# Kernel tuning notes

Measured on AMD Instinct MI355X. Metric: run time of the kernel, lower is better.

## Reference

```python
import jax, jax.numpy as jnp
import numpy as np

D_MODEL = 1024
NUM_HEADS = 16
HEAD_DIM = D_MODEL // NUM_HEADS
THETA = 10000.0
B, S = 2, 2048


def setup_inputs() -> dict:
    key = jax.random.key(0)
    ks = jax.random.split(key, 9)
    std = 1.0 / np.sqrt(D_MODEL)
    x = jax.random.normal(ks[0], (B, S, D_MODEL), dtype=jnp.float32)
    Wq = jax.random.normal(ks[1], (D_MODEL, D_MODEL), dtype=jnp.float32) * std
    Wk = jax.random.normal(ks[2], (D_MODEL, D_MODEL), dtype=jnp.float32) * std
    Wv = jax.random.normal(ks[3], (D_MODEL, D_MODEL), dtype=jnp.float32) * std
    Wo = jax.random.normal(ks[4], (D_MODEL, D_MODEL), dtype=jnp.float32) * std
    bq = jax.random.normal(ks[5], (D_MODEL,), dtype=jnp.float32) * std
    bk = jax.random.normal(ks[6], (D_MODEL,), dtype=jnp.float32) * std
    bv = jax.random.normal(ks[7], (D_MODEL,), dtype=jnp.float32) * std
    bo = jax.random.normal(ks[8], (D_MODEL,), dtype=jnp.float32) * std
    return {"x": x, "Wq": Wq, "bq": bq, "Wk": Wk, "bk": bk,
            "Wv": Wv, "bv": bv, "Wo": Wo, "bo": bo}


def _apply_rope(t, cos, sin):
    # t: [B, H, S, hd]; cos/sin: [S, hd//2]; interleaved-pair rotation
    t1 = t[..., 0::2]
    t2 = t[..., 1::2]
    r1 = t1 * cos - t2 * sin
    r2 = t1 * sin + t2 * cos
    return jnp.stack([r1, r2], axis=-1).reshape(t.shape)


def reference(x, Wq, bq, Wk, bk, Wv, bv, Wo, bo):
    B_, S_, D = x.shape
    H, hd = NUM_HEADS, HEAD_DIM
    # QKV projections (nn.Linear: x @ W.T + b)
    q = (x @ Wq.T + bq).reshape(B_, S_, H, hd).transpose(0, 2, 1, 3)  # [B,H,S,hd]
    k = (x @ Wk.T + bk).reshape(B_, S_, H, hd).transpose(0, 2, 1, 3)
    v = (x @ Wv.T + bv).reshape(B_, S_, H, hd).transpose(0, 2, 1, 3)
    # RoPE with token_positions = arange(S)
    pos = jnp.arange(S_, dtype=jnp.float32)
    inv_freq = 1.0 / (THETA ** (jnp.arange(0, hd, 2, dtype=jnp.float32) / hd))
    ang = pos[:, None] * inv_freq[None, :]  # [S, hd//2]
    cos, sin = jnp.cos(ang), jnp.sin(ang)
    q = _apply_rope(q, cos, sin)
    k = _apply_rope(k, cos, sin)
    # causal scaled-dot-product attention
    scores = jnp.einsum('bhqd,bhkd->bhqk', q, k) / jnp.sqrt(jnp.asarray(hd, x.dtype))
    causal = jnp.arange(S_)[:, None] >= jnp.arange(S_)[None, :]  # [S,S]
    scores = jnp.where(causal, scores, -jnp.inf)
    attn = jax.nn.softmax(scores, axis=-1)
    out = jnp.einsum('bhqk,bhkd->bhqd', attn, v)  # [B,H,S,hd]
    out = out.transpose(0, 2, 1, 3).reshape(B_, S_, D)
    return out @ Wo.T + bo
```

## Files before the change

### kernel.cpp

```cpp
#include <hip/hip_runtime.h>
#include <hip/hip_bf16.h>
#include <stdint.h>

typedef __bf16 bf16_t;
typedef __bf16 bf16x4 __attribute__((ext_vector_type(4)));
typedef __bf16 bf16x8 __attribute__((ext_vector_type(8)));
typedef float  f32x4  __attribute__((ext_vector_type(4)));

#define DM    1024
#define NH    16
#define HD    64
#define SEQ   2048
#define BATCH 2
#define BS    (BATCH*SEQ)
#define NQKV  (3*DM)

#define GLOAD_LDS16(g, l) \
  __builtin_amdgcn_global_load_lds((const __attribute__((address_space(1))) void*)(g), \
                                   (__attribute__((address_space(3))) void*)(l), 16, 0, 0)

__device__ __forceinline__ f32x4 mfma16(bf16x8 a, bf16x8 b, f32x4 c) {
  return __builtin_amdgcn_mfma_f32_16x16x32_bf16(a, b, c, 0, 0, 0);
}

__global__ __launch_bounds__(256) void k_cast_all(
    const float* __restrict__ x,  const float* __restrict__ Wq,
    const float* __restrict__ Wk, const float* __restrict__ Wv,
    const float* __restrict__ Wo, const float* __restrict__ bq,
    const float* __restrict__ bk, const float* __restrict__ bv,
    bf16_t* __restrict__ xb, bf16_t* __restrict__ Wcat,
    bf16_t* __restrict__ Wob, float* __restrict__ bcat,
    float2* __restrict__ rt)
{
  const int bid = blockIdx.x, tid = threadIdx.x;
  if (bid >= 4099) {
    const int idx = (bid - 4099) * 256 + tid;
    const int s = idx >> 5, i = idx & 31;
    float inv = powf(10000.0f, -(float)(2 * i) / 64.0f);
    float ang = (float)s * inv;
    rt[idx] = make_float2(cosf(ang), sinf(ang));
    return;
  }
  if (bid >= 4096) {
    const int k = bid - 4096;
    const float* src = (k == 0) ? bq : (k == 1) ? bk : bv;
    *(float4*)&bcat[k * DM + tid * 4] = *(const float4*)&src[tid * 4];
    return;
  }
  const float* src; bf16_t* dst; int i;
  if (bid < 2048)      { src = x;  dst = xb;                i = bid * 2048 + tid * 8; }
  else if (bid < 2560) { src = Wq; dst = Wcat;              i = (bid - 2048) * 2048 + tid * 8; }
  else if (bid < 3072) { src = Wk; dst = Wcat + DM * DM;    i = (bid - 2560) * 2048 + tid * 8; }
  else if (bid < 3584) { src = Wv; dst = Wcat + 2 * DM * DM;i = (bid - 3072) * 2048 + tid * 8; }
  else                 { src = Wo; dst = Wob;               i = (bid - 3584) * 2048 + tid * 8; }
  float4 a = *(const float4*)(src + i);
  float4 b = *(const float4*)(src + i + 4);
  bf16x8 o;
  o[0] = (bf16_t)a.x; o[1] = (bf16_t)a.y; o[2] = (bf16_t)a.z; o[3] = (bf16_t)a.w;
  o[4] = (bf16_t)b.x; o[5] = (bf16_t)b.y; o[6] = (bf16_t)b.z; o[7] = (bf16_t)b.w;
  *(bf16x8*)(dst + i) = o;
}

__global__ __launch_bounds__(256) void k_gemm_qk(
    const bf16_t* __restrict__ A, const bf16_t* __restrict__ B,
    const float* __restrict__ bias, const float2* __restrict__ rt,
    bf16_t* __restrict__ Qo, bf16_t* __restrict__ Ko)
{
  const int K = DM;
  __shared__ __align__(16) bf16_t As[128 * 32];
  __shared__ __align__(16) bf16_t Bs[128 * 32];
  const int tid  = threadIdx.x;
  const int lane = tid & 63;
  const int wave = tid >> 6;
  const int wr = wave >> 1, wc = wave & 1;
  const int m0 = blockIdx.y * 128, n0 = blockIdx.x * 128;
  const int c16 = lane & 15, g = lane >> 4;

  f32x4 acc[4][4];
  #pragma unroll
  for (int i = 0; i < 4; ++i)
    #pragma unroll
    for (int j = 0; j < 4; ++j)
      #pragma unroll
      for (int e = 0; e < 4; ++e) acc[i][j][e] = 0.0f;

  const int srow = wave * 32;
  const int lrow = lane >> 2;
  const int lk   = (lane & 3) * 8;
  const bf16_t* ga0 = A + (size_t)(m0 + srow +      lrow) * K + lk;
  const bf16_t* ga1 = A + (size_t)(m0 + srow + 16 + lrow) * K + lk;
  const bf16_t* gb0 = B + (size_t)(n0 + srow +      lrow) * K + lk;
  const bf16_t* gb1 = B + (size_t)(n0 + srow + 16 + lrow) * K + lk;
  bf16_t* la0 = &As[(srow)      * 32];
  bf16_t* la1 = &As[(srow + 16) * 32];
  bf16_t* lb0 = &Bs[(srow)      * 32];
  bf16_t* lb1 = &Bs[(srow + 16) * 32];

  const bf16_t* pa = &As[(wr * 64 + c16) * 32 + g * 8];
  const bf16_t* pb = &Bs[(wc * 64 + c16) * 32 + g * 8];

  for (int kt = 0; kt < K; kt += 32) {
    GLOAD_LDS16(ga0 + kt, la0);
    GLOAD_LDS16(ga1 + kt, la1);
    GLOAD_LDS16(gb0 + kt, lb0);
    GLOAD_LDS16(gb1 + kt, lb1);
    __syncthreads();
    bf16x8 af[4], bfr[4];
    #pragma unroll
    for (int t = 0; t < 4; ++t) af[t]  = *(const bf16x8*)(pa + t * 16 * 32);
    #pragma unroll
    for (int t = 0; t < 4; ++t) bfr[t] = *(const bf16x8*)(pb + t * 16 * 32);
    #pragma unroll
    for (int i = 0; i < 4; ++i)
      #pragma unroll
      for (int j = 0; j < 4; ++j)
        acc[i][j] = mfma16(bfr[j], af[i], acc[i][j]);
    __syncthreads();
  }

  const int region = n0 >> 10;
  bf16_t* dst = region ? Ko : Qo;
  const float qs = region ? 1.0f : (0.125f * 1.44269504088896f);
  #pragma unroll
  for (int j = 0; j < 4; ++j) {
    const int nb = n0 + wc * 64 + j * 16 + (g << 2);
    const float4 bv = *(const float4*)&bias[nb];
    const int h  = (nb >> 6) & 15;
    const int d0 = nb & 63;
    #pragma unroll
    for (int i = 0; i < 4; ++i) {
      const int m = m0 + wr * 64 + i * 16 + c16;
      const int s = m & 2047;
      const int bh = ((m >> 11) << 4) + h;
      const float4 cs = *(const float4*)&rt[(size_t)s * 32 + (d0 >> 1)];
      const float v0 = acc[i][j][0] + bv.x;
      const float v1 = acc[i][j][1] + bv.y;
      const float v2 = acc[i][j][2] + bv.z;
      const float v3 = acc[i][j][3] + bv.w;
      bf16x4 ov;
      ov[0] = (bf16_t)((v0 * cs.x - v1 * cs.y) * qs);
      ov[1] = (bf16_t)((v0 * cs.y + v1 * cs.x) * qs);
      ov[2] = (bf16_t)((v2 * cs.z - v3 * cs.w) * qs);
      ov[3] = (bf16_t)((v2 * cs.w + v3 * cs.z) * qs);
      *(bf16x4*)&dst[((size_t)bh * SEQ + s) * HD + d0] = ov;
    }
  }
}

__global__ __launch_bounds__(256) void k_gemm_v(
    const bf16_t* __restrict__ A, const bf16_t* __restrict__ B,
    const float* __restrict__ bias, bf16_t* __restrict__ Vt)
{
  const int K = DM;
  __shared__ __align__(16) bf16_t As[128 * 32];
  __shared__ __align__(16) bf16_t Bs[128 * 32];
  const int tid  = threadIdx.x;
  const int lane = tid & 63;
  const int wave = tid >> 6;
  const int wr = wave >> 1, wc = wave & 1;
  const int m0 = blockIdx.y * 128, n0 = blockIdx.x * 128;
  const int c16 = lane & 15, g = lane >> 4;

  f32x4 acc[4][4];
  #pragma unroll
  for (int i = 0; i < 4; ++i)
    #pragma unroll
    for (int j = 0; j < 4; ++j)
      #pragma unroll
      for (int e = 0; e < 4; ++e) acc[i][j][e] = 0.0f;

  const int srow = wave * 32;
  const int lrow = lane >> 2;
  const int lk   = (lane & 3) * 8;
  const bf16_t* ga0 = A + (size_t)(m0 + srow +      lrow) * K + lk;
  const bf16_t* ga1 = A + (size_t)(m0 + srow + 16 + lrow) * K + lk;
  const bf16_t* gb0 = B + (size_t)(n0 + srow +      lrow) * K + lk;
  const bf16_t* gb1 = B + (size_t)(n0 + srow + 16 + lrow) * K + lk;
  bf16_t* la0 = &As[(srow)      * 32];
  bf16_t* la1 = &As[(srow + 16) * 32];
  bf16_t* lb0 = &Bs[(srow)      * 32];
  bf16_t* lb1 = &Bs[(srow + 16) * 32];

  const bf16_t* pa = &As[(wr * 64 + c16) * 32 + g * 8];
  const bf16_t* pb = &Bs[(wc * 64 + c16) * 32 + g * 8];

  for (int kt = 0; kt < K; kt += 32) {
    GLOAD_LDS16(ga0 + kt, la0);
    GLOAD_LDS16(ga1 + kt, la1);
    GLOAD_LDS16(gb0 + kt, lb0);
    GLOAD_LDS16(gb1 + kt, lb1);
    __syncthreads();
    bf16x8 af[4], bfr[4];
    #pragma unroll
    for (int t = 0; t < 4; ++t) af[t]  = *(const bf16x8*)(pa + t * 16 * 32);
    #pragma unroll
    for (int t = 0; t < 4; ++t) bfr[t] = *(const bf16x8*)(pb + t * 16 * 32);
    #pragma unroll
    for (int i = 0; i < 4; ++i)
      #pragma unroll
      for (int j = 0; j < 4; ++j)
        acc[i][j] = mfma16(af[i], bfr[j], acc[i][j]);
    __syncthreads();
  }

  const int rbase = m0 + wr * 64 + (g << 2);
  const int cbase = n0 + wc * 64 + c16;
  #pragma unroll
  for (int j = 0; j < 4; ++j) {
    const int c = cbase + j * 16;
    const float bv = bias[c];
    const int h = (c >> 6) & 15;
    const int d = c & 63;
    #pragma unroll
    for (int i = 0; i < 4; ++i) {
      bf16x4 ov;
      #pragma unroll
      for (int e = 0; e < 4; ++e) ov[e] = (bf16_t)(acc[i][j][e] + bv);
      const int r0 = rbase + i * 16;
      const int bh = ((r0 >> 11) << 4) + h;
      const int s0 = r0 & 2047;
      const int u  = (s0 >> 4) & 3;
      const int p0 = (s0 & ~63) + ((u >> 1) << 5) + (g << 3) + ((u & 1) << 2);
      *(bf16x4*)&Vt[((size_t)bh * HD + d) * SEQ + p0] = ov;
    }
  }
}

__global__ __launch_bounds__(512) void k_gemm_out(
    const bf16_t* __restrict__ A, const bf16_t* __restrict__ B,
    const float* __restrict__ bias, float* __restrict__ C)
{
  const int K = DM, N = DM;
  __shared__ __align__(16) bf16_t As[128 * 32];
  __shared__ __align__(16) bf16_t Bs[128 * 32];
  const int tid  = threadIdx.x;
  const int lane = tid & 63;
  const int w    = tid >> 6;
  const int wr = w >> 2, wc = w & 3;
  const int m0 = blockIdx.y * 128, n0 = blockIdx.x * 128;
  const int c16 = lane & 15, g = lane >> 4;

  f32x4 acc[4][2];
  #pragma unroll
  for (int i = 0; i < 4; ++i)
    #pragma unroll
    for (int j = 0; j < 2; ++j)
      #pragma unroll
      for (int e = 0; e < 4; ++e) acc[i][j][e] = 0.0f;

  const int lrow = lane >> 2;
  const int lk   = (lane & 3) * 8;
  const bf16_t* ga = A + (size_t)(m0 + w * 16 + lrow) * K + lk;
  const bf16_t* gb = B + (size_t)(n0 + w * 16 + lrow) * K + lk;
  bf16_t* la = &As[(w * 16) * 32];
  bf16_t* lb = &Bs[(w * 16) * 32];

  const bf16_t* pa = &As[(wr * 64 + c16) * 32 + g * 8];
  const bf16_t* pb = &Bs[(wc * 32 + c16) * 32 + g * 8];

  for (int kt = 0; kt < K; kt += 32) {
    GLOAD_LDS16(ga + kt, la);
    GLOAD_LDS16(gb + kt, lb);
    __syncthreads();
    bf16x8 af[4], bfr[2];
    #pragma unroll
    for (int t = 0; t < 4; ++t) af[t]  = *(const bf16x8*)(pa + t * 16 * 32);
    #pragma unroll
    for (int t = 0; t < 2; ++t) bfr[t] = *(const bf16x8*)(pb + t * 16 * 32);
    #pragma unroll
    for (int i = 0; i < 4; ++i)
      #pragma unroll
      for (int j = 0; j < 2; ++j)
        acc[i][j] = mfma16(af[i], bfr[j], acc[i][j]);
    __syncthreads();
  }

  const int rbase = m0 + wr * 64 + (g << 2);
  const int cbase = n0 + wc * 32 + c16;
  #pragma unroll
  for (int j = 0; j < 2; ++j) {
    const int c = cbase + j * 16;
    const float bv = bias[c];
    #pragma unroll
    for (int i = 0; i < 4; ++i) {
      #pragma unroll
      for (int e = 0; e < 4; ++e) {
        const int r = rbase + i * 16 + e;
        C[(size_t)r * N + c] = acc[i][j][e] + bv;
      }
    }
  }
}

__global__ __launch_bounds__(256, 4) void k_attn(
    const bf16_t* __restrict__ Q, const bf16_t* __restrict__ K,
    const bf16_t* __restrict__ Vt, bf16_t* __restrict__ O)
{
  __shared__ __align__(16) bf16_t kbuf[2][64 * 64];
  __shared__ __align__(16) bf16_t vbuf[2][64 * 64];
  const int tid = threadIdx.x, lane = tid & 63, w = tid >> 6;
  const int rr = blockIdx.x >> 8;
  const int kk = (blockIdx.x >> 5) & 7;
  const int bh = blockIdx.x & 31;
  const int qt = (rr == 0) ? kk : (rr == 1) ? 15 - kk : (rr == 2) ? 16 + kk : 31 - kk;
  const int b  = bh >> 4, h = bh & 15;
  const int q0 = qt * 64 + w * 16;
  const int c16 = lane & 15;
  const int g   = lane >> 4;
  const int q   = q0 + c16;

  const bf16_t* Qb = Q  + (size_t)bh * SEQ * HD;
  const bf16_t* Kb = K  + (size_t)bh * SEQ * HD;
  const bf16_t* Vb = Vt + (size_t)bh * HD * SEQ;

  bf16x8 qf0 = *(const bf16x8*)&Qb[(size_t)q * HD + g * 8];
  bf16x8 qf1 = *(const bf16x8*)&Qb[(size_t)q * HD + 32 + g * 8];

  f32x4 oacc[4];
  #pragma unroll
  for (int dblk = 0; dblk < 4; ++dblk)
    #pragma unroll
    for (int e = 0; e < 4; ++e) oacc[dblk][e] = 0.0f;
  float m_ = -1e30f, l_ = 0.0f;

  const int ntile = qt + 1;

  const int soff0 = w * 1024 + lane * 16;
  const int soff1 = soff0 + 4096;
  const int srow0 = soff0 >> 7, srow1 = soff1 >> 7;
  const int scb0  = (soff0 & 127) ^ ((srow0 & 7) << 4);
  const int scb1  = (soff1 & 127) ^ ((srow1 & 7) << 4);
  const bf16_t* gk0 = &Kb[(size_t)srow0 * HD + (scb0 >> 1)];
  const bf16_t* gk1 = &Kb[(size_t)srow1 * HD + (scb1 >> 1)];
  const bf16_t* gv0 = &Vb[(size_t)srow0 * SEQ + (scb0 >> 1)];
  const bf16_t* gv1 = &Vb[(size_t)srow1 * SEQ + (scb1 >> 1)];
  bf16_t* lk0A = &kbuf[0][(w * 1024) >> 1];
  bf16_t* lk1A = &kbuf[0][(w * 1024 + 4096) >> 1];
  bf16_t* lk0B = &kbuf[1][(w * 1024) >> 1];
  bf16_t* lk1B = &kbuf[1][(w * 1024 + 4096) >> 1];
  bf16_t* lv0A = &vbuf[0][(w * 1024) >> 1];
  bf16_t* lv1A = &vbuf[0][(w * 1024 + 4096) >> 1];
  bf16_t* lv0B = &vbuf[1][(w * 1024) >> 1];
  bf16_t* lv1B = &vbuf[1][(w * 1024 + 4096) >> 1];

  const int sw = (c16 & 7) << 4;
  const int e0 = ((16 * g) ^ sw) >> 1;
  const int dhi = (((64 + 16 * g) ^ sw) >> 1) - e0;
  const bf16_t* kp0 = &kbuf[0][c16 * 64 + e0];
  const bf16_t* kp1 = &kbuf[1][c16 * 64 + e0];
  const bf16_t* vp0 = &vbuf[0][c16 * 64 + e0];
  const bf16_t* vp1 = &vbuf[1][c16 * 64 + e0];

  GLOAD_LDS16(gk0, lk0A); GLOAD_LDS16(gk1, lk1A);
  GLOAD_LDS16(gv0, lv0A); GLOAD_LDS16(gv1, lv1A);
  gk0 += 4096; gk1 += 4096; gv0 += 64; gv1 += 64;
  __syncthreads();

  for (int t = 0; t < ntile; ++t) {
    const bool odd = t & 1;
    if (t + 1 < ntile) {
      GLOAD_LDS16(gk0, odd ? lk0A : lk0B); GLOAD_LDS16(gk1, odd ? lk1A : lk1B);
      GLOAD_LDS16(gv0, odd ? lv0A : lv0B); GLOAD_LDS16(gv1, odd ? lv1A : lv1B);
      gk0 += 4096; gk1 += 4096; gv0 += 64; gv1 += 64;
    }

    const bf16_t* kp = odd ? kp1 : kp0;
    const bf16_t* vp = odd ? vp1 : vp0;

    f32x4 st[4];
    __builtin_amdgcn_s_setprio(1);
    #pragma unroll
    for (int u = 0; u < 4; ++u) {
      bf16x8 k0 = *(const bf16x8*)(kp + u * 1024);
      bf16x8 k1 = *(const bf16x8*)(kp + u * 1024 + dhi);
      f32x4 z; z[0] = z[1] = z[2] = z[3] = 0.0f;
      z = mfma16(k0, qf0, z);
      z = mfma16(k1, qf1, z);
      st[u] = z;
    }
    __builtin_amdgcn_s_setprio(0);

    bf16x8 vlo[4], vhi[4];
    #pragma unroll
    for (int dblk = 0; dblk < 4; ++dblk) {
      vlo[dblk] = *(const bf16x8*)(vp + dblk * 1024);
      vhi[dblk] = *(const bf16x8*)(vp + dblk * 1024 + dhi);
    }

    float pv[16];
    if (t == qt) {
      const int kv0 = t * 64;
      #pragma unroll
      for (int u = 0; u < 4; ++u)
        #pragma unroll
        for (int r = 0; r < 4; ++r) {
          const int kv = kv0 + 16 * u + 4 * g + r;
          pv[u * 4 + r] = (kv <= q) ? st[u][r] : -1e30f;
        }
    } else {
      #pragma unroll
      for (int u = 0; u < 4; ++u)
        #pragma unroll
        for (int r = 0; r < 4; ++r)
          pv[u * 4 + r] = st[u][r];
    }

    float ma = fmaxf(fmaxf(pv[0], pv[1]), fmaxf(pv[2], pv[3]));
    float mb = fmaxf(fmaxf(pv[4], pv[5]), fmaxf(pv[6], pv[7]));
    float mc = fmaxf(fmaxf(pv[8], pv[9]), fmaxf(pv[10], pv[11]));
    float md = fmaxf(fmaxf(pv[12], pv[13]), fmaxf(pv[14], pv[15]));
    const float lmx = fmaxf(fmaxf(ma, mb), fmaxf(mc, md));

    if (__any(lmx - m_ > 12.0f)) {
      float mx = fmaxf(lmx, __shfl_xor(lmx, 16));
      mx = fmaxf(mx, __shfl_xor(mx, 32));
      const float mn = fmaxf(m_, mx);
      const float alpha = exp2f(m_ - mn);
      l_ *= alpha;
      #pragma unroll
      for (int dblk = 0; dblk < 4; ++dblk)
        #pragma unroll
        for (int e = 0; e < 4; ++e) oacc[dblk][e] *= alpha;
      m_ = mn;
    }

    #pragma unroll
    for (int i = 0; i < 16; ++i) pv[i] = exp2f(pv[i] - m_);
    float s0 = (pv[0] + pv[1]) + (pv[2] + pv[3]);
    float s1 = (pv[4] + pv[5]) + (pv[6] + pv[7]);
    float s2 = (pv[8] + pv[9]) + (pv[10] + pv[11]);
    float s3 = (pv[12] + pv[13]) + (pv[14] + pv[15]);
    l_ += (s0 + s1) + (s2 + s3);

    bf16x8 pf0, pf1;
    #pragma unroll
    for (int j = 0; j < 8; ++j) {
      pf0[j] = (bf16_t)pv[j];
      pf1[j] = (bf16_t)pv[8 + j];
    }

    __builtin_amdgcn_s_setprio(1);
    #pragma unroll
    for (int dblk = 0; dblk < 4; ++dblk) {
      oacc[dblk] = mfma16(vlo[dblk], pf0, oacc[dblk]);
      oacc[dblk] = mfma16(vhi[dblk], pf1, oacc[dblk]);
    }
    __builtin_amdgcn_s_setprio(0);

    __syncthreads();
  }

  l_ += __shfl_xor(l_, 16);
  l_ += __shfl_xor(l_, 32);
  const float inv = 1.0f / l_;
  bf16_t* orow = O + ((size_t)(b * SEQ + q)) * DM + h * HD;
  #pragma unroll
  for (int dblk = 0; dblk < 4; ++dblk) {
    bf16x4 ov;
    #pragma unroll
    for (int r = 0; r < 4; ++r) ov[r] = (bf16_t)(oacc[dblk][r] * inv);
    *(bf16x4*)&orow[dblk * 16 + 4 * g] = ov;
  }
}

extern "C" void kernel_launch(void* const* d_in, const int* in_sizes, int n_in,
                              void* d_out, int out_size, void* d_ws, size_t ws_size,
                              hipStream_t stream)
{
  const float* x  = (const float*)d_in[0];
  const float* Wq = (const float*)d_in[1];
  const float* bq = (const float*)d_in[2];
  const float* Wk = (const float*)d_in[3];
  const float* bk = (const float*)d_in[4];
  const float* Wv = (const float*)d_in[5];
  const float* bv = (const float*)d_in[6];
  const float* Wo = (const float*)d_in[7];
  const float* bo = (const float*)d_in[8];
  float* out = (float*)d_out;

  char* ws = (char*)d_ws;
  size_t off = 0;
  auto alloc = [&](size_t bytes) { char* p = ws + off; off += (bytes + 255) & ~255ULL; return p; };
  bf16_t* xb   = (bf16_t*)alloc((size_t)BS * DM * 2);
  bf16_t* Wcat = (bf16_t*)alloc((size_t)NQKV * DM * 2);
  bf16_t* Wob  = (bf16_t*)alloc((size_t)DM * DM * 2);
  float*  bcat = (float*)alloc((size_t)NQKV * 4);
  float2* rt   = (float2*)alloc((size_t)SEQ * 32 * 8);
  bf16_t* Qh   = (bf16_t*)alloc((size_t)BS * DM * 2);
  bf16_t* Kh   = (bf16_t*)alloc((size_t)BS * DM * 2);
  bf16_t* Vth  = (bf16_t*)alloc((size_t)BS * DM * 2);
  bf16_t* Oh   = (bf16_t*)alloc((size_t)BS * DM * 2);
  (void)ws_size; (void)in_sizes; (void)n_in; (void)out_size;

  k_cast_all<<<4099 + 256, 256, 0, stream>>>(x, Wq, Wk, Wv, Wo, bq, bk, bv,
                                             xb, Wcat, Wob, bcat, rt);

  dim3 gqk(16, 32);
  k_gemm_qk<<<gqk, 256, 0, stream>>>(xb, Wcat, bcat, rt, Qh, Kh);
  dim3 gv(8, 32);
  k_gemm_v<<<gv, 256, 0, stream>>>(xb, Wcat + 2 * DM * DM, bcat + 2 * DM, Vth);
  k_attn<<<32 * 32, 256, 0, stream>>>(Qh, Kh, Vth, Oh);
  dim3 g2(DM / 128, BS / 128);
  k_gemm_out<<<g2, 512, 0, stream>>>(Oh, Wob, bo, out);
}
```

Before: 126.8 us.

## Split attention KV tiles across wave pairs and shrink query tile to 32 rows

```diff
diff --git a/kernel.cpp b/kernel.cpp
--- a/kernel.cpp
+++ b/kernel.cpp
@@ -292,21 +292,25 @@
   }
 }
 
-__global__ __launch_bounds__(256, 4) void k_attn(
+__global__ __launch_bounds__(256, 8) void k_attn(
     const bf16_t* __restrict__ Q, const bf16_t* __restrict__ K,
     const bf16_t* __restrict__ Vt, bf16_t* __restrict__ O)
 {
-  __shared__ __align__(16) bf16_t kbuf[2][64 * 64];
-  __shared__ __align__(16) bf16_t vbuf[2][64 * 64];
+  __shared__ __align__(16) unsigned char smem[16384];
+  bf16_t* kb0 = (bf16_t*)smem;
+  bf16_t* kb1 = kb0 + 2048;
+  bf16_t* vb0 = kb1 + 2048;
+  bf16_t* vb1 = vb0 + 2048;
+
   const int tid = threadIdx.x, lane = tid & 63, w = tid >> 6;
+  const int bh = blockIdx.x & 31;
+  const int kk = (blockIdx.x >> 5) & 7;
   const int rr = blockIdx.x >> 8;
-  const int kk = (blockIdx.x >> 5) & 7;
-  const int bh = blockIdx.x & 31;
-  const int qt = (rr == 0) ? kk : (rr == 1) ? 15 - kk : (rr == 2) ? 16 + kk : 31 - kk;
+  const int qt = rr * 8 + ((rr & 1) ? 7 - kk : kk);
   const int b  = bh >> 4, h = bh & 15;
-  const int q0 = qt * 64 + w * 16;
-  const int c16 = lane & 15;
-  const int g   = lane >> 4;
+  const int rg = w & 1, par = w >> 1;
+  const int q0 = qt * 32 + rg * 16;
+  const int c16 = lane & 15, g = lane >> 4;
   const int q   = q0 + c16;
 
   const bf16_t* Qb = Q  + (size_t)bh * SEQ * HD;
@@ -323,143 +327,139 @@
     for (int e = 0; e < 4; ++e) oacc[dblk][e] = 0.0f;
   float m_ = -1e30f, l_ = 0.0f;
 
-  const int ntile = qt + 1;
-
-  const int soff0 = w * 1024 + lane * 16;
-  const int soff1 = soff0 + 4096;
-  const int srow0 = soff0 >> 7, srow1 = soff1 >> 7;
-  const int scb0  = (soff0 & 127) ^ ((srow0 & 7) << 4);
-  const int scb1  = (soff1 & 127) ^ ((srow1 & 7) << 4);
-  const bf16_t* gk0 = &Kb[(size_t)srow0 * HD + (scb0 >> 1)];
-  const bf16_t* gk1 = &Kb[(size_t)srow1 * HD + (scb1 >> 1)];
-  const bf16_t* gv0 = &Vb[(size_t)srow0 * SEQ + (scb0 >> 1)];
-  const bf16_t* gv1 = &Vb[(size_t)srow1 * SEQ + (scb1 >> 1)];
-  bf16_t* lk0A = &kbuf[0][(w * 1024) >> 1];
-  bf16_t* lk1A = &kbuf[0][(w * 1024 + 4096) >> 1];
-  bf16_t* lk0B = &kbuf[1][(w * 1024) >> 1];
-  bf16_t* lk1B = &kbuf[1][(w * 1024 + 4096) >> 1];
-  bf16_t* lv0A = &vbuf[0][(w * 1024) >> 1];
-  bf16_t* lv1A = &vbuf[0][(w * 1024 + 4096) >> 1];
-  bf16_t* lv0B = &vbuf[1][(w * 1024) >> 1];
-  bf16_t* lv1B = &vbuf[1][(w * 1024 + 4096) >> 1];
-
-  const int sw = (c16 & 7) << 4;
-  const int e0 = ((16 * g) ^ sw) >> 1;
-  const int dhi = (((64 + 16 * g) ^ sw) >> 1) - e0;
-  const bf16_t* kp0 = &kbuf[0][c16 * 64 + e0];
-  const bf16_t* kp1 = &kbuf[1][c16 * 64 + e0];
-  const bf16_t* vp0 = &vbuf[0][c16 * 64 + e0];
-  const bf16_t* vp1 = &vbuf[1][c16 * 64 + e0];
-
-  GLOAD_LDS16(gk0, lk0A); GLOAD_LDS16(gk1, lk1A);
-  GLOAD_LDS16(gv0, lv0A); GLOAD_LDS16(gv1, lv1A);
-  gk0 += 4096; gk1 += 4096; gv0 += 64; gv1 += 64;
+  const int T = qt + 1;
+
+  const int soff  = w * 1024 + lane * 16;
+  const int krow  = soff >> 7;
+  const int kcolb = (soff & 127) ^ ((krow & 7) << 4);
+  const int vrow  = soff >> 6;
+  const int vcolb = (soff & 63) ^ (((vrow >> 1) & 3) << 4);
+  const bf16_t* gk = &Kb[(size_t)krow * HD + (kcolb >> 1)];
+  const bf16_t* gv = &Vb[(size_t)vrow * SEQ + (vcolb >> 1)];
+  bf16_t* kD0 = kb0 + ((w * 1024) >> 1);
+  bf16_t* kD1 = kb1 + ((w * 1024) >> 1);
+  bf16_t* vD0 = vb0 + ((w * 1024) >> 1);
+  bf16_t* vD1 = vb1 + ((w * 1024) >> 1);
+
+  const int e0  = ((16 * g) ^ ((c16 & 7) << 4)) >> 1;
+  const int dhi = (((64 + 16 * g) ^ ((c16 & 7) << 4)) >> 1) - e0;
+  const bf16_t* kp = (par ? kb1 : kb0) + c16 * 64 + e0;
+  const int ve  = ((16 * g) ^ (((c16 >> 1) & 3) << 4)) >> 1;
+  const bf16_t* vp = (par ? vb1 : vb0) + c16 * 32 + ve;
+
+  GLOAD_LDS16(gk, kD0); GLOAD_LDS16(gv, vD0);
+  gk += 32 * HD; gv += 32;
   __syncthreads();
 
-  for (int t = 0; t < ntile; ++t) {
-    const bool odd = t & 1;
-    if (t + 1 < ntile) {
-      GLOAD_LDS16(gk0, odd ? lk0A : lk0B); GLOAD_LDS16(gk1, odd ? lk1A : lk1B);
-      GLOAD_LDS16(gv0, odd ? lv0A : lv0B); GLOAD_LDS16(gv1, odd ? lv1A : lv1B);
-      gk0 += 4096; gk1 += 4096; gv0 += 64; gv1 += 64;
+  for (int t = 0; t < T; ++t) {
+    if (t + 1 < T) {
+      const bool nb = (t + 1) & 1;
+      GLOAD_LDS16(gk, nb ? kD1 : kD0);
+      GLOAD_LDS16(gv, nb ? vD1 : vD0);
+      gk += 32 * HD; gv += 32;
     }
 
-    const bf16_t* kp = odd ? kp1 : kp0;
-    const bf16_t* vp = odd ? vp1 : vp0;
-
-    f32x4 st[4];
-    __builtin_amdgcn_s_setprio(1);
-    #pragma unroll
-    for (int u = 0; u < 4; ++u) {
-      bf16x8 k0 = *(const bf16x8*)(kp + u * 1024);
-      bf16x8 k1 = *(const bf16x8*)(kp + u * 1024 + dhi);
-      f32x4 z; z[0] = z[1] = z[2] = z[3] = 0.0f;
-      z = mfma16(k0, qf0, z);
-      z = mfma16(k1, qf1, z);
-      st[u] = z;
+    if ((t & 1) == par) {
+      f32x4 st[2];
+      __builtin_amdgcn_s_setprio(1);
+      #pragma unroll
+      for (int u = 0; u < 2; ++u) {
+        bf16x8 k0 = *(const bf16x8*)(kp + u * 1024);
+        bf16x8 k1 = *(const bf16x8*)(kp + u * 1024 + dhi);
+        f32x4 z; z[0] = z[1] = z[2] = z[3] = 0.0f;
+        z = mfma16(k0, qf0, z);
+        z = mfma16(k1, qf1, z);
+        st[u] = z;
+      }
+      __builtin_amdgcn_s_setprio(0);
+
+      bf16x8 vf[4];
+      #pragma unroll
+      for (int dblk = 0; dblk < 4; ++dblk)
+        vf[dblk] = *(const bf16x8*)(vp + dblk * 512);
+
+      float pv[8];
+      if (t == qt) {
+        const int kv0 = t * 32;
+        #pragma unroll
+        for (int u = 0; u < 2; ++u)
+          #pragma unroll
+          for (int r = 0; r < 4; ++r) {
+            const int kv = kv0 + 16 * u + 4 * g + r;
+            pv[u * 4 + r] = (kv <= q) ? st[u][r] : -1e30f;
+          }
+      } else {
+        #pragma unroll
+        for (int u = 0; u < 2; ++u)
+          #pragma unroll
+          for (int r = 0; r < 4; ++r)
+            pv[u * 4 + r] = st[u][r];
+      }
+
+      float ma = fmaxf(fmaxf(pv[0], pv[1]), fmaxf(pv[2], pv[3]));
+      float mb = fmaxf(fmaxf(pv[4], pv[5]), fmaxf(pv[6], pv[7]));
+      const float lmx = fmaxf(ma, mb);
+
+      if (__any(lmx - m_ > 12.0f)) {
+        float mx = fmaxf(lmx, __shfl_xor(lmx, 16));
+        mx = fmaxf(mx, __shfl_xor(mx, 32));
+        const float mn = fmaxf(m_, mx);
+        const float alpha = exp2f(m_ - mn);
+        l_ *= alpha;
+        #pragma unroll
+        for (int dblk = 0; dblk < 4; ++dblk)
+          #pragma unroll
+          for (int e = 0; e < 4; ++e) oacc[dblk][e] *= alpha;
+        m_ = mn;
+      }
+
+      #pragma unroll
+      for (int i = 0; i < 8; ++i) pv[i] = exp2f(pv[i] - m_);
+      l_ += ((pv[0] + pv[1]) + (pv[2] + pv[3])) + ((pv[4] + pv[5]) + (pv[6] + pv[7]));
+
+      bf16x8 pf0;
+      #pragma unroll
+      for (int j = 0; j < 8; ++j) pf0[j] = (bf16_t)pv[j];
+
+      __builtin_amdgcn_s_setprio(1);
+      #pragma unroll
+      for (int dblk = 0; dblk < 4; ++dblk)
+        oacc[dblk] = mfma16(vf[dblk], pf0, oacc[dblk]);
+      __builtin_amdgcn_s_setprio(0);
     }
-    __builtin_amdgcn_s_setprio(0);
-
-    bf16x8 vlo[4], vhi[4];
+
+    __syncthreads();
+  }
+
+  float* comb = (float*)smem;
+  if (par == 1) {
+    float* cpd = comb + (rg * 64 + lane) * 18;
+    cpd[0] = m_; cpd[1] = l_;
+    #pragma unroll
+    for (int dblk = 0; dblk < 4; ++dblk)
+      #pragma unroll
+      for (int e = 0; e < 4; ++e) cpd[2 + dblk * 4 + e] = oacc[dblk][e];
+  }
+  __syncthreads();
+  if (par == 0) {
+    const float* cps = comb + (rg * 64 + lane) * 18;
+    const float m2 = cps[0], l2 = cps[1];
+    const float M  = fmaxf(m_, m2);
+    const float a1 = exp2f(m_ - M);
+    const float a2 = exp2f(m2 - M);
+    float l = a1 * l_ + a2 * l2;
+    l += __shfl_xor(l, 16);
+    l += __shfl_xor(l, 32);
+    const float inv = 1.0f / l;
+    bf16_t* orow = O + ((size_t)(b * SEQ + q)) * DM + h * HD;
     #pragma unroll
     for (int dblk = 0; dblk < 4; ++dblk) {
-      vlo[dblk] = *(const bf16x8*)(vp + dblk * 1024);
-      vhi[dblk] = *(const bf16x8*)(vp + dblk * 1024 + dhi);
+      bf16x4 ov;
+      #pragma unroll
+      for (int r = 0; r < 4; ++r)
+        ov[r] = (bf16_t)((a1 * oacc[dblk][r] + a2 * cps[2 + dblk * 4 + r]) * inv);
+      *(bf16x4*)&orow[dblk * 16 + 4 * g] = ov;
     }
-
-    float pv[16];
-    if (t == qt) {
-      const int kv0 = t * 64;
-      #pragma unroll
-      for (int u = 0; u < 4; ++u)
-        #pragma unroll
-        for (int r = 0; r < 4; ++r) {
-          const int kv = kv0 + 16 * u + 4 * g + r;
-          pv[u * 4 + r] = (kv <= q) ? st[u][r] : -1e30f;
-        }
-    } else {
-      #pragma unroll
-      for (int u = 0; u < 4; ++u)
-        #pragma unroll
-        for (int r = 0; r < 4; ++r)
-          pv[u * 4 + r] = st[u][r];
-    }
-
-    float ma = fmaxf(fmaxf(pv[0], pv[1]), fmaxf(pv[2], pv[3]));
-    float mb = fmaxf(fmaxf(pv[4], pv[5]), fmaxf(pv[6], pv[7]));
-    float mc = fmaxf(fmaxf(pv[8], pv[9]), fmaxf(pv[10], pv[11]));
-    float md = fmaxf(fmaxf(pv[12], pv[13]), fmaxf(pv[14], pv[15]));
-    const float lmx = fmaxf(fmaxf(ma, mb), fmaxf(mc, md));
-
-    if (__any(lmx - m_ > 12.0f)) {
-      float mx = fmaxf(lmx, __shfl_xor(lmx, 16));
-      mx = fmaxf(mx, __shfl_xor(mx, 32));
-      const float mn = fmaxf(m_, mx);
-      const float alpha = exp2f(m_ - mn);
-      l_ *= alpha;
-      #pragma unroll
-      for (int dblk = 0; dblk < 4; ++dblk)
-        #pragma unroll
-        for (int e = 0; e < 4; ++e) oacc[dblk][e] *= alpha;
-      m_ = mn;
-    }
-
-    #pragma unroll
-    for (int i = 0; i < 16; ++i) pv[i] = exp2f(pv[i] - m_);
-    float s0 = (pv[0] + pv[1]) + (pv[2] + pv[3]);
-    float s1 = (pv[4] + pv[5]) + (pv[6] + pv[7]);
-    float s2 = (pv[8] + pv[9]) + (pv[10] + pv[11]);
-    float s3 = (pv[12] + pv[13]) + (pv[14] + pv[15]);
-    l_ += (s0 + s1) + (s2 + s3);
-
-    bf16x8 pf0, pf1;
-    #pragma unroll
-    for (int j = 0; j < 8; ++j) {
-      pf0[j] = (bf16_t)pv[j];
-      pf1[j] = (bf16_t)pv[8 + j];
-    }
-
-    __builtin_amdgcn_s_setprio(1);
-    #pragma unroll
-    for (int dblk = 0; dblk < 4; ++dblk) {
-      oacc[dblk] = mfma16(vlo[dblk], pf0, oacc[dblk]);
-      oacc[dblk] = mfma16(vhi[dblk], pf1, oacc[dblk]);
-    }
-    __builtin_amdgcn_s_setprio(0);
-
-    __syncthreads();
-  }
-
-  l_ += __shfl_xor(l_, 16);
-  l_ += __shfl_xor(l_, 32);
-  const float inv = 1.0f / l_;
-  bf16_t* orow = O + ((size_t)(b * SEQ + q)) * DM + h * HD;
-  #pragma unroll
-  for (int dblk = 0; dblk < 4; ++dblk) {
-    bf16x4 ov;
-    #pragma unroll
-    for (int r = 0; r < 4; ++r) ov[r] = (bf16_t)(oacc[dblk][r] * inv);
-    *(bf16x4*)&orow[dblk * 16 + 4 * g] = ov;
   }
 }
 
@@ -499,7 +499,7 @@
   k_gemm_qk<<<gqk, 256, 0, stream>>>(xb, Wcat, bcat, rt, Qh, Kh);
   dim3 gv(8, 32);
   k_gemm_v<<<gv, 256, 0, stream>>>(xb, Wcat + 2 * DM * DM, bcat + 2 * DM, Vth);
-  k_attn<<<32 * 32, 256, 0, stream>>>(Qh, Kh, Vth, Oh);
+  k_attn<<<2048, 256, 0, stream>>>(Qh, Kh, Vth, Oh);
   dim3 g2(DM / 128, BS / 128);
   k_gemm_out<<<g2, 512, 0, stream>>>(Oh, Wob, bo, out);
 }
```

After: 154.6 us. +22.0%, slower.
